# Performance work log

Hardware: AMD Instinct MI355X
Metric: run time of the kernel (lower is better)

Reference implementation:

```python
import jax, jax.numpy as jnp
import numpy as np

CUTOFF = 1.0          # nm, PhysNet attenuation cutoff
KE = 138.96           # Coulomb constant in kJ/mol*nm/e^2
N_ATOMS = 245760
N_PAIRS = 16_777_216
N_MOLS = 4096


def physnet_attenuation(r):
    # PhysNet smooth cutoff: 1 - 6u^5 + 15u^4 - 10u^3 for u = r/cutoff < 1, else 0
    u = r / CUTOFF
    phi = 1.0 - 6.0 * u**5 + 15.0 * u**4 - 10.0 * u**3
    return jnp.where(u < 1.0, phi, 0.0)


def setup_inputs() -> dict:
    key = jax.random.key(0)
    k1, k2, k3, k4 = jax.random.split(key, 4)
    per_atom_charge = jax.random.normal(k1, (N_ATOMS,), dtype=jnp.float32) * 0.2
    raw = jax.random.randint(k2, (2, N_PAIRS), 0, N_ATOMS, dtype=jnp.int32)
    # enforce idx_i <= idx_j; equal pairs are dropped by the idx_i < idx_j mask
    pair_indices = jnp.stack([jnp.minimum(raw[0], raw[1]), jnp.maximum(raw[0], raw[1])])
    # distances in (0.05, 1.5) nm to avoid div-by-zero and span the cutoff
    d_ij = jax.random.uniform(k3, (N_PAIRS, 1), dtype=jnp.float32) * 1.45 + 0.05
    atomic_subsystem_indices = jax.random.randint(k4, (N_PAIRS,), 0, N_MOLS, dtype=jnp.int32)
    per_system_energy = jnp.zeros((N_MOLS,), dtype=jnp.float32)
    return {
        "per_atom_charge": per_atom_charge,
        "pair_indices": pair_indices,
        "d_ij": d_ij,
        "atomic_subsystem_indices": atomic_subsystem_indices,
        "per_system_energy": per_system_energy,
    }


def reference(per_atom_charge, pair_indices, d_ij, atomic_subsystem_indices, per_system_energy):
    idx_i = pair_indices[0]
    idx_j = pair_indices[1]
    unique_mask = idx_i < idx_j  # keep each pair once (static-shape masking via where)
    d = d_ij[:, 0]  # [P]
    phi_2r = physnet_attenuation(2.0 * d)
    # cutoff-blended Coulomb kernel chi(r)
    chi_r = phi_2r / jnp.sqrt(d * d + 1.0) + (1.0 - phi_2r) / d
    contrib = per_atom_charge[idx_i] * per_atom_charge[idx_j] * chi_r
    contrib = jnp.where(unique_mask, contrib, 0.0)
    energy = per_system_energy + jax.ops.segment_sum(
        contrib, atomic_subsystem_indices, num_segments=N_MOLS
    )
    return energy * KE
```

## Files before the change

### kernel.cpp

```cpp
#include <hip/hip_runtime.h>

static constexpr int   NPAIRS = 16777216;
static constexpr int   NMOLS  = 4096;
static constexpr float KEF    = 138.96f;
static constexpr int   TPB    = 256;
static constexpr int   BLOCKS = 1024;

__global__ __launch_bounds__(TPB) void zero_out_kernel(float* __restrict__ out) {
    int i = blockIdx.x * TPB + threadIdx.x;
    if (i < NMOLS) out[i] = 0.0f;
}

__device__ __forceinline__ float pair_contrib(const float* __restrict__ q,
                                              int i, int j, float d) {
    float u = 2.0f * d;
    float phi = 0.0f;
    if (u < 1.0f) {
        phi = 1.0f - u * u * u * (10.0f + u * (6.0f * u - 15.0f));
    }
    float chi = phi * rsqrtf(d * d + 1.0f) + (1.0f - phi) / d;
    float c = q[i] * q[j] * chi;
    return (i < j) ? c : 0.0f;
}

__global__ __launch_bounds__(TPB) void coulomb_kernel(
    const float* __restrict__ q,
    const int*   __restrict__ pidx,
    const float* __restrict__ dij,
    const int*   __restrict__ mol,
    float*       __restrict__ out)
{
    __shared__ float bins[NMOLS];
    for (int i = threadIdx.x; i < NMOLS; i += TPB) bins[i] = 0.0f;
    __syncthreads();

    const int4*   pi4 = (const int4*)pidx;
    const int4*   pj4 = (const int4*)(pidx + NPAIRS);
    const float4* d4  = (const float4*)dij;
    const int4*   m4  = (const int4*)mol;

    const int nvec   = NPAIRS / 4;
    const int stride = gridDim.x * TPB;
    for (int v = blockIdx.x * TPB + threadIdx.x; v < nvec; v += stride) {
        int4   ii = pi4[v];
        int4   jj = pj4[v];
        float4 dd = d4[v];
        int4   mm = m4[v];

        float c0 = pair_contrib(q, ii.x, jj.x, dd.x);
        float c1 = pair_contrib(q, ii.y, jj.y, dd.y);
        float c2 = pair_contrib(q, ii.z, jj.z, dd.z);
        float c3 = pair_contrib(q, ii.w, jj.w, dd.w);

        atomicAdd(&bins[mm.x], c0);
        atomicAdd(&bins[mm.y], c1);
        atomicAdd(&bins[mm.z], c2);
        atomicAdd(&bins[mm.w], c3);
    }

    __syncthreads();
    for (int i = threadIdx.x; i < NMOLS; i += TPB) {
        atomicAdd(&out[i], bins[i]);
    }
}

__global__ __launch_bounds__(TPB) void finalize_kernel(float* __restrict__ out,
                                                       const float* __restrict__ pse) {
    int i = blockIdx.x * TPB + threadIdx.x;
    if (i < NMOLS) out[i] = (out[i] + pse[i]) * KEF;
}

extern "C" void kernel_launch(void* const* d_in, const int* in_sizes, int n_in,
                              void* d_out, int out_size, void* d_ws, size_t ws_size,
                              hipStream_t stream) {
    const float* q    = (const float*)d_in[0];
    const int*   pidx = (const int*)  d_in[1];
    const float* dij  = (const float*)d_in[2];
    const int*   mol  = (const int*)  d_in[3];
    const float* pse  = (const float*)d_in[4];
    float* out = (float*)d_out;

    zero_out_kernel<<<NMOLS / TPB, TPB, 0, stream>>>(out);
    coulomb_kernel<<<BLOCKS, TPB, 0, stream>>>(q, pidx, dij, mol, out);
    finalize_kernel<<<NMOLS / TPB, TPB, 0, stream>>>(out, pse);
}
```

Measured before the change: 388.3 us.

## Stage streaming pair loads through LDS via global_load_lds and double grid size

Streams the four per-pair input arrays into shared memory with direct global-to-LDS loads, waits on vmcnt, then reads each lane's vector back from LDS. It also doubles the block count to 2048 with a fixed iteration count, and swaps rsqrt and divide for the hardware approximate rsq/rcp builtins. The aim is to cut register pressure and raise the number of memory requests in flight. In exchange it adds an LDS round trip, a full vmcnt(0) stall every iteration with no prefetch, and slightly less precise reciprocal results.

```diff
diff --git a/kernel.cpp b/kernel.cpp
--- a/kernel.cpp
+++ b/kernel.cpp
@@ -4,11 +4,21 @@
 static constexpr int   NMOLS  = 4096;
 static constexpr float KEF    = 138.96f;
 static constexpr int   TPB    = 256;
-static constexpr int   BLOCKS = 1024;
+static constexpr int   BLOCKS = 2048;
+static constexpr int   WAVES  = TPB / 64;
+static constexpr int   NITER  = NPAIRS / 4 / (BLOCKS * TPB);
 
-__global__ __launch_bounds__(TPB) void zero_out_kernel(float* __restrict__ out) {
-    int i = blockIdx.x * TPB + threadIdx.x;
+typedef int   vi4 __attribute__((ext_vector_type(4)));
+typedef float vf4 __attribute__((ext_vector_type(4)));
+
+__global__ __launch_bounds__(256) void zero_out_kernel(float* __restrict__ out) {
+    int i = blockIdx.x * 256 + threadIdx.x;
     if (i < NMOLS) out[i] = 0.0f;
+}
+
+__device__ __forceinline__ void stage16(const void* gptr, void* lptr) {
+    __builtin_amdgcn_global_load_lds((const unsigned int*)gptr, (unsigned int*)lptr,
+                                     16, 0, 0);
 }
 
 __device__ __forceinline__ float pair_contrib(const float* __restrict__ q,
@@ -18,7 +28,9 @@
     if (u < 1.0f) {
         phi = 1.0f - u * u * u * (10.0f + u * (6.0f * u - 15.0f));
     }
-    float chi = phi * rsqrtf(d * d + 1.0f) + (1.0f - phi) / d;
+    float rs = __builtin_amdgcn_rsqf(d * d + 1.0f);
+    float rd = __builtin_amdgcn_rcpf(d);
+    float chi = phi * rs + (1.0f - phi) * rd;
     float c = q[i] * q[j] * chi;
     return (i < j) ? c : 0.0f;
 }
@@ -31,21 +43,32 @@
     float*       __restrict__ out)
 {
     __shared__ float bins[NMOLS];
+    __shared__ vi4   stage[WAVES][4][64];
     for (int i = threadIdx.x; i < NMOLS; i += TPB) bins[i] = 0.0f;
     __syncthreads();
 
-    const int4*   pi4 = (const int4*)pidx;
-    const int4*   pj4 = (const int4*)(pidx + NPAIRS);
-    const float4* d4  = (const float4*)dij;
-    const int4*   m4  = (const int4*)mol;
+    const vi4* pi4 = (const vi4*)pidx;
+    const vi4* pj4 = (const vi4*)(pidx + NPAIRS);
+    const vf4* d4  = (const vf4*)dij;
+    const vi4* m4  = (const vi4*)mol;
 
-    const int nvec   = NPAIRS / 4;
-    const int stride = gridDim.x * TPB;
-    for (int v = blockIdx.x * TPB + threadIdx.x; v < nvec; v += stride) {
-        int4   ii = pi4[v];
-        int4   jj = pj4[v];
-        float4 dd = d4[v];
-        int4   mm = m4[v];
+    const int lane   = threadIdx.x & 63;
+    const int wave   = threadIdx.x >> 6;
+    const int stride = BLOCKS * TPB;
+    int v = blockIdx.x * TPB + threadIdx.x;
+
+    #pragma unroll 1
+    for (int k = 0; k < NITER; ++k, v += stride) {
+        stage16(&pi4[v], &stage[wave][0][0]);
+        stage16(&pj4[v], &stage[wave][1][0]);
+        stage16(&d4[v],  &stage[wave][2][0]);
+        stage16(&m4[v],  &stage[wave][3][0]);
+        asm volatile("s_waitcnt vmcnt(0)" ::: "memory");
+
+        vi4 ii = stage[wave][0][lane];
+        vi4 jj = stage[wave][1][lane];
+        vf4 dd = (vf4)stage[wave][2][lane];
+        vi4 mm = stage[wave][3][lane];
 
         float c0 = pair_contrib(q, ii.x, jj.x, dd.x);
         float c1 = pair_contrib(q, ii.y, jj.y, dd.y);
@@ -64,9 +87,9 @@
     }
 }
 
-__global__ __launch_bounds__(TPB) void finalize_kernel(float* __restrict__ out,
+__global__ __launch_bounds__(256) void finalize_kernel(float* __restrict__ out,
                                                        const float* __restrict__ pse) {
-    int i = blockIdx.x * TPB + threadIdx.x;
+    int i = blockIdx.x * 256 + threadIdx.x;
     if (i < NMOLS) out[i] = (out[i] + pse[i]) * KEF;
 }
 
@@ -80,7 +103,7 @@
     const float* pse  = (const float*)d_in[4];
     float* out = (float*)d_out;
 
-    zero_out_kernel<<<NMOLS / TPB, TPB, 0, stream>>>(out);
+    zero_out_kernel<<<NMOLS / 256, 256, 0, stream>>>(out);
     coulomb_kernel<<<BLOCKS, TPB, 0, stream>>>(q, pidx, dij, mol, out);
-    finalize_kernel<<<NMOLS / TPB, TPB, 0, stream>>>(out, pse);
+    finalize_kernel<<<NMOLS / 256, 256, 0, stream>>>(out, pse);
 }
```

After: 381.0 us. Within noise of the previous version (-1.9%).
